# Kernel optimization log

Hardware: AMD Instinct MI355X
Metric: run time of the kernel (lower is better)

Reference implementation:

```python
import jax, jax.numpy as jnp
import numpy as np

EPS = 1e-12  # matches torch F.normalize default eps


def setup_inputs() -> dict:
    key = jax.random.key(0)
    k1, = jax.random.split(key, 1)
    N, M, D = 1024, 40, 768
    x = jax.random.normal(k1, (N, M, D), dtype=jnp.float32)
    w = jnp.asarray(15.0, dtype=jnp.float32)
    b = jnp.asarray(-7.0, dtype=jnp.float32)
    return {"x": x, "w": w, "b": b}


def reference(x, w, b):
    N, M, D = x.shape
    # L2 normalize along feature dim (torch F.normalize: x / max(||x||, eps))
    norm = jnp.linalg.norm(x, axis=-1, keepdims=True)
    xn = x / jnp.maximum(norm, EPS)
    # Inclusive centroids [N, D]
    c_incl = jnp.mean(xn, axis=1)
    # Exclusive centroids [N, M, D]: leave-one-out mean
    c_excl = (M * c_incl[:, None, :] - xn) / (M - 1)
    # Similarity of every utterance to every inclusive centroid: [N, M, N]
    sim = jnp.einsum('nmd,kd->nmk', xn, c_incl)
    # Own-speaker column uses the exclusive centroid instead (vectorized
    # replacement of the per-speaker diagonal-block loop)
    diag = jnp.sum(xn * c_excl, axis=-1)                 # [N, M]
    own = jnp.eye(N, dtype=bool)[:, None, :]             # [N, 1, N]
    sim = jnp.where(own, diag[:, :, None], sim)
    # Affine scale then cross-entropy against speaker labels
    logits = (w * sim + b).reshape(N * M, N)
    labels = jnp.repeat(jnp.arange(N), M)                # [N*M]
    lse = jax.nn.logsumexp(logits, axis=-1)
    picked = jnp.take_along_axis(logits, labels[:, None], axis=1)[:, 0]
    loss = jnp.mean(lse - picked)
    return loss
```

## Files before the change

kernel.cpp:

```cpp
#include <hip/hip_runtime.h>
#include <hip/hip_bf16.h>
#include <hip/hip_fp8.h>

typedef float f32x4 __attribute__((ext_vector_type(4)));
typedef long long i64;
typedef i64 i64x2 __attribute__((ext_vector_type(2)));

#define N_SPK 1024
#define M_UTT 40
#define D_FEAT 768
#define NROWS (N_SPK * M_UTT)
#define LOG2E 1.44269504088896340736f
#define LN2   0.69314718055994530942f

#define BM 128
#define BN 128
#define BKB 64
#define KT (D_FEAT / BKB)
#define ROWB 768

#define INV_SS (1.0f / 64.0f)
#define SCL 8.0f

__device__ __forceinline__ unsigned char to_fp8(float v) {
  __hip_fp8_e4m3 t(v);
  return (unsigned char)t.__x;
}


__global__ __launch_bounds__(256) void k_norm_cent(const float* __restrict__ x,
                                                   unsigned char* __restrict__ xn,
                                                   unsigned char* __restrict__ cc) {
  const int n = blockIdx.x, t = threadIdx.x;
  const float* xb = x + (size_t)n * (M_UTT * D_FEAT);
  unsigned char* ob = xn + (size_t)n * (M_UTT * D_FEAT);
  const int lane = t & 63, wv = t >> 6;
  const int j  = t & 63;
  const int pj = ((j >> 3) & 3) * 16 + (j & 7) + ((j >> 5) << 3);
  const int s0 = (t & ~63) + pj;
  __shared__ float wsum[2][2][4];
  float c0 = 0.f, c1 = 0.f, c2 = 0.f;
  for (int m = 0; m < M_UTT; m += 2) {
    const int p = (m >> 1) & 1;
    const float* r0 = xb + (size_t)m * D_FEAT;
    const float* r1 = r0 + D_FEAT;
    float a0 = r0[t], a1 = r0[t + 256], a2 = r0[t + 512];
    float b0 = r1[t], b1 = r1[t + 256], b2 = r1[t + 512];
    float sq0 = a0 * a0 + a1 * a1 + a2 * a2;
    float sq1 = b0 * b0 + b1 * b1 + b2 * b2;
#pragma unroll
    for (int d = 1; d < 64; d <<= 1) {
      sq0 += __shfl_xor(sq0, d, 64);
      sq1 += __shfl_xor(sq1, d, 64);
    }
    if (lane == 0) { wsum[p][0][wv] = sq0; wsum[p][1][wv] = sq1; }
    __syncthreads();
    const float t0 = wsum[p][0][0] + wsum[p][0][1] + wsum[p][0][2] + wsum[p][0][3];
    const float t1 = wsum[p][1][0] + wsum[p][1][1] + wsum[p][1][2] + wsum[p][1][3];
    const float i0 = 1.0f / fmaxf(sqrtf(t0), 1e-12f);
    const float i1 = 1.0f / fmaxf(sqrtf(t1), 1e-12f);
    a0 *= i0; a1 *= i0; a2 *= i0;
    b0 *= i1; b1 *= i1; b2 *= i1;
    unsigned char* o0 = ob + (size_t)m * D_FEAT;
    unsigned char* o1 = o0 + D_FEAT;
    o0[s0] = to_fp8(a0 * SCL); o0[s0 + 256] = to_fp8(a1 * SCL); o0[s0 + 512] = to_fp8(a2 * SCL);
    o1[s0] = to_fp8(b0 * SCL); o1[s0 + 256] = to_fp8(b1 * SCL); o1[s0 + 512] = to_fp8(b2 * SCL);
    c0 += a0 + b0; c1 += a1 + b1; c2 += a2 + b2;
  }
  unsigned char* co = cc + (size_t)n * D_FEAT;
  co[s0]       = to_fp8(c0 * (SCL / M_UTT));
  co[s0 + 256] = to_fp8(c1 * (SCL / M_UTT));
  co[s0 + 512] = to_fp8(c2 * (SCL / M_UTT));
}

#define GLD(g, l) __builtin_amdgcn_global_load_lds( \
    (const __attribute__((address_space(1))) unsigned int*)(g), \
    (__attribute__((address_space(3))) unsigned int*)(l), 16, 0, 0)

__global__ __launch_bounds__(256, 4) void k_gemm_part(
    const unsigned char* __restrict__ XN, const unsigned char* __restrict__ CC,
    const float* __restrict__ wp, const float* __restrict__ bp,
    float2* __restrict__ ppart, float* __restrict__ picked2) {

  __shared__ __align__(16) char smem[32768];

  const int tid  = threadIdx.x;
  const int wave = tid >> 6, lane = tid & 63;
  const int l16  = lane & 15, lg = lane >> 4;
  const int wr   = wave >> 1, wc = wave & 1;

  const int bid = blockIdx.x;
  const int xcd = bid & 7;
  const int tt  = bid >> 3;
  const int rb  = xcd * 40 + (tt >> 3);
  const int cb  = tt & 7;
  const int rowbase = rb * BM;
  const int colbase = cb * BN;

  const int R7   = (tid >> 3) & 7;
  const int li   = ((tid & 7) * 16) ^ (R7 << 4);
  const int row0 = 2 * (tid >> 3) + (li >> 6);
  const int kb   = li & 63;
  const int t16  = tid * 16;
  const unsigned char* gA = XN + (size_t)(rowbase + row0) * ROWB + kb;
  const unsigned char* gB = CC + (size_t)(colbase + row0) * ROWB + kb;

  const int xr  = ((l16 >> 1) & 7) << 4;
  const int in0 = ((((l16 & 1) << 6) | (lg << 4)) ^ xr);
  int aoff[4], boff[4];
#pragma unroll
  for (int i = 0; i < 4; ++i) {
    aoff[i] = (wr * 32 + i * 8 + (l16 >> 1)) * 128 + in0;
    boff[i] = 8192 + (wc * 32 + i * 8 + (l16 >> 1)) * 128 + in0;
  }

  f32x4 acc[4][4];
#pragma unroll
  for (int i = 0; i < 4; ++i)
#pragma unroll
    for (int jj = 0; jj < 4; ++jj) acc[i][jj] = (f32x4){0.f, 0.f, 0.f, 0.f};

  auto STAGE = [&](int buf, int koff) {
    char* sb = smem + buf * 16384;
    GLD(gA + koff,              sb + t16);
    GLD(gA + 64 * ROWB + koff,  sb + 4096 + t16);
    GLD(gB + koff,              sb + 8192 + t16);
    GLD(gB + 64 * ROWB + koff,  sb + 12288 + t16);
  };

  STAGE(0, 0);

  for (int k = 0; k < KT; ++k) {
    const char* bb = smem + (k & 1) * 16384;
    if (k + 1 < KT) {
      STAGE((k + 1) & 1, (k + 1) * BKB);
      asm volatile("s_waitcnt vmcnt(4)" ::: "memory");
    } else {
      asm volatile("s_waitcnt vmcnt(0)" ::: "memory");
    }
    __builtin_amdgcn_s_barrier();

    i64x2 av[4], bv[4];
#pragma unroll
    for (int i = 0; i < 4; ++i) av[i] = *(const i64x2*)(bb + aoff[i]);
#pragma unroll
    for (int jj = 0; jj < 4; ++jj) bv[jj] = *(const i64x2*)(bb + boff[jj]);
    __builtin_amdgcn_s_setprio(1);
#pragma unroll
    for (int i = 0; i < 4; ++i)
#pragma unroll
      for (int jj = 0; jj < 4; ++jj)
        acc[i][jj] = __builtin_amdgcn_mfma_f32_16x16x32_fp8_fp8(av[i][0], bv[jj][0], acc[i][jj], 0, 0, 0);
#pragma unroll
    for (int i = 0; i < 4; ++i)
#pragma unroll
      for (int jj = 0; jj < 4; ++jj)
        acc[i][jj] = __builtin_amdgcn_mfma_f32_16x16x32_fp8_fp8(av[i][1], bv[jj][1], acc[i][jj], 0, 0, 0);
    __builtin_amdgcn_s_setprio(0);
    asm volatile("s_waitcnt lgkmcnt(0)" ::: "memory");
    __builtin_amdgcn_s_barrier();
  }

  const float ws2 = wp[0] * LOG2E;
  const float b2  = bp[0] * LOG2E;
  float2* red = (float2*)smem;

#pragma unroll
  for (int i = 0; i < 4; ++i) {
#pragma unroll
    for (int rr = 0; rr < 4; ++rr) {
      const int lrow = wr * 64 + i * 16 + lg * 4 + rr;
      const int R = rowbase + lrow;
      const int n = R / M_UTT;
      float l2[4];
#pragma unroll
      for (int jj = 0; jj < 4; ++jj) {
        float sim = acc[i][jj][rr] * INV_SS;
        const int gc = colbase + wc * 64 + jj * 16 + l16;
        if (gc == n) {
          sim = (40.f * sim - 1.f) * (1.f / 39.f);
          picked2[R] = fmaf(ws2, sim, b2);
        }
        l2[jj] = fmaf(ws2, sim, b2);
      }
      float mx = fmaxf(fmaxf(l2[0], l2[1]), fmaxf(l2[2], l2[3]));
#pragma unroll
      for (int d = 1; d < 16; d <<= 1) mx = fmaxf(mx, __shfl_xor(mx, d, 64));
      float s = exp2f(l2[0] - mx) + exp2f(l2[1] - mx) +
                exp2f(l2[2] - mx) + exp2f(l2[3] - mx);
#pragma unroll
      for (int d = 1; d < 16; d <<= 1) s += __shfl_xor(s, d, 64);
      if (l16 == 0) red[lrow * 2 + wc] = make_float2(mx, s);
    }
  }
  __syncthreads();
  if (tid < 128) {
    const float2 p0 = red[tid * 2 + 0];
    const float2 p1 = red[tid * 2 + 1];
    const float m2 = fmaxf(p0.x, p1.x);
    const float ss = p0.y * exp2f(p0.x - m2) + p1.y * exp2f(p1.x - m2);
    ppart[(size_t)(rowbase + tid) * 8 + cb] = make_float2(m2, ss);
  }
}

__global__ __launch_bounds__(256) void k_combine(const float2* __restrict__ pp,
                                                 const float* __restrict__ picked2,
                                                 float* __restrict__ rowloss) {
  const int R = blockIdx.x * 256 + threadIdx.x;
  const float2* p = pp + (size_t)R * 8;
  float2 v[8];
#pragma unroll
  for (int j = 0; j < 8; ++j) v[j] = p[j];
  float m2 = v[0].x;
#pragma unroll
  for (int j = 1; j < 8; ++j) m2 = fmaxf(m2, v[j].x);
  float s = 0.f;
#pragma unroll
  for (int j = 0; j < 8; ++j) s += v[j].y * exp2f(v[j].x - m2);
  const float lse2 = m2 + log2f(s);
  rowloss[R] = (lse2 - picked2[R]) * LN2;
}

__global__ __launch_bounds__(512) void k_reduce(const float* __restrict__ rowloss,
                                                float* __restrict__ out) {
  const int t = threadIdx.x;
  double s = 0.0;
  for (int i = t; i < NROWS; i += 512) s += (double)rowloss[i];
  __shared__ double sm[512];
  sm[t] = s;
  __syncthreads();
  for (int off = 256; off > 0; off >>= 1) {
    if (t < off) sm[t] += sm[t + off];
    __syncthreads();
  }
  if (t == 0) out[0] = (float)(sm[0] / (double)NROWS);
}

extern "C" void kernel_launch(void* const* d_in, const int* in_sizes, int n_in,
                              void* d_out, int out_size, void* d_ws, size_t ws_size,
                              hipStream_t stream) {
  const float* x = (const float*)d_in[0];
  const float* w = (const float*)d_in[1];
  const float* b = (const float*)d_in[2];
  char* ws = (char*)d_ws;
  size_t off = 0;
  unsigned char* xn = (unsigned char*)(ws + off); off += (size_t)NROWS * D_FEAT;
  unsigned char* cc = (unsigned char*)(ws + off); off += (size_t)N_SPK * D_FEAT;
  off = (off + 255) & ~(size_t)255;
  float2* ppart      = (float2*)(ws + off);        off += (size_t)NROWS * 8 * sizeof(float2);
  float* picked2     = (float*)(ws + off);         off += (size_t)NROWS * sizeof(float);
  float* rowloss     = (float*)(ws + off);         off += (size_t)NROWS * sizeof(float);
  float* out = (float*)d_out;

  k_norm_cent<<<N_SPK, 256, 0, stream>>>(x, xn, cc);
  k_gemm_part<<<(NROWS / BM) * (N_SPK / BN), 256, 0, stream>>>(xn, cc, w, b, ppart, picked2);
  k_combine<<<NROWS / 256, 256, 0, stream>>>(ppart, picked2, rowloss);
  k_reduce<<<1, 512, 0, stream>>>(rowloss, out);
}
```

Baseline: 114.5 us.

## Switch GEMM to scaled 16x16x128 FP8 MFMA with 128-byte K tiles

Replaces pairs of 16x16x32 FP8 MFMAs with the gfx950 scaled 16x16x128 f8f6f4 MFMA using unit scales. The K tile doubles to 128 bytes and LDS grows to 64 KB with a new XOR swizzle, and the norm kernel now writes FP8 rows in natural order instead of pre-permuted. The goal is fewer MFMA issues, fewer loop iterations and fewer barriers. In exchange, occupancy drops from 4 to 2 blocks per CU, and the new layout and swizzle must stay consistent with the operand format the instruction expects.

After: 316.9 us. +176.8%, slower.

```diff
diff --git a/kernel.cpp b/kernel.cpp
--- a/kernel.cpp
+++ b/kernel.cpp
@@ -3,8 +3,8 @@
 #include <hip/hip_fp8.h>
 
 typedef float f32x4 __attribute__((ext_vector_type(4)));
-typedef long long i64;
-typedef i64 i64x2 __attribute__((ext_vector_type(2)));
+typedef int   i32x4 __attribute__((ext_vector_type(4)));
+typedef int   i32x8 __attribute__((ext_vector_type(8)));
 
 #define N_SPK 1024
 #define M_UTT 40
@@ -15,18 +15,18 @@
 
 #define BM 128
 #define BN 128
-#define BKB 64
+#define BKB 128
 #define KT (D_FEAT / BKB)
 #define ROWB 768
 
 #define INV_SS (1.0f / 64.0f)
 #define SCL 8.0f
+#define SCALE1 0x7F7F7F7F
 
 __device__ __forceinline__ unsigned char to_fp8(float v) {
   __hip_fp8_e4m3 t(v);
   return (unsigned char)t.__x;
 }
-
 
 __global__ __launch_bounds__(256) void k_norm_cent(const float* __restrict__ x,
                                                    unsigned char* __restrict__ xn,
@@ -35,9 +35,6 @@
   const float* xb = x + (size_t)n * (M_UTT * D_FEAT);
   unsigned char* ob = xn + (size_t)n * (M_UTT * D_FEAT);
   const int lane = t & 63, wv = t >> 6;
-  const int j  = t & 63;
-  const int pj = ((j >> 3) & 3) * 16 + (j & 7) + ((j >> 5) << 3);
-  const int s0 = (t & ~63) + pj;
   __shared__ float wsum[2][2][4];
   float c0 = 0.f, c1 = 0.f, c2 = 0.f;
   for (int m = 0; m < M_UTT; m += 2) {
@@ -63,26 +60,26 @@
     b0 *= i1; b1 *= i1; b2 *= i1;
     unsigned char* o0 = ob + (size_t)m * D_FEAT;
     unsigned char* o1 = o0 + D_FEAT;
-    o0[s0] = to_fp8(a0 * SCL); o0[s0 + 256] = to_fp8(a1 * SCL); o0[s0 + 512] = to_fp8(a2 * SCL);
-    o1[s0] = to_fp8(b0 * SCL); o1[s0 + 256] = to_fp8(b1 * SCL); o1[s0 + 512] = to_fp8(b2 * SCL);
+    o0[t] = to_fp8(a0 * SCL); o0[t + 256] = to_fp8(a1 * SCL); o0[t + 512] = to_fp8(a2 * SCL);
+    o1[t] = to_fp8(b0 * SCL); o1[t + 256] = to_fp8(b1 * SCL); o1[t + 512] = to_fp8(b2 * SCL);
     c0 += a0 + b0; c1 += a1 + b1; c2 += a2 + b2;
   }
   unsigned char* co = cc + (size_t)n * D_FEAT;
-  co[s0]       = to_fp8(c0 * (SCL / M_UTT));
-  co[s0 + 256] = to_fp8(c1 * (SCL / M_UTT));
-  co[s0 + 512] = to_fp8(c2 * (SCL / M_UTT));
+  co[t]       = to_fp8(c0 * (SCL / M_UTT));
+  co[t + 256] = to_fp8(c1 * (SCL / M_UTT));
+  co[t + 512] = to_fp8(c2 * (SCL / M_UTT));
 }
 
 #define GLD(g, l) __builtin_amdgcn_global_load_lds( \
     (const __attribute__((address_space(1))) unsigned int*)(g), \
     (__attribute__((address_space(3))) unsigned int*)(l), 16, 0, 0)
 
-__global__ __launch_bounds__(256, 4) void k_gemm_part(
+__global__ __launch_bounds__(256, 2) void k_gemm_part(
     const unsigned char* __restrict__ XN, const unsigned char* __restrict__ CC,
     const float* __restrict__ wp, const float* __restrict__ bp,
     float2* __restrict__ ppart, float* __restrict__ picked2) {
 
-  __shared__ __align__(16) char smem[32768];
+  __shared__ __align__(16) char smem[65536];
 
   const int tid  = threadIdx.x;
   const int wave = tid >> 6, lane = tid & 63;
@@ -97,21 +94,19 @@
   const int rowbase = rb * BM;
   const int colbase = cb * BN;
 
-  const int R7   = (tid >> 3) & 7;
-  const int li   = ((tid & 7) * 16) ^ (R7 << 4);
-  const int row0 = 2 * (tid >> 3) + (li >> 6);
-  const int kb   = li & 63;
+  const int row0 = tid >> 3;
+  const int u    = (tid & 7) ^ ((tid >> 3) & 7);
   const int t16  = tid * 16;
-  const unsigned char* gA = XN + (size_t)(rowbase + row0) * ROWB + kb;
-  const unsigned char* gB = CC + (size_t)(colbase + row0) * ROWB + kb;
-
-  const int xr  = ((l16 >> 1) & 7) << 4;
-  const int in0 = ((((l16 & 1) << 6) | (lg << 4)) ^ xr);
+  const unsigned char* gA = XN + (size_t)(rowbase + row0) * ROWB + u * 16;
+  const unsigned char* gB = CC + (size_t)(colbase + row0) * ROWB + u * 16;
+
+  const int m7 = l16 & 7;
+  const int s0 = ((2 * lg) ^ m7) << 4;
   int aoff[4], boff[4];
 #pragma unroll
   for (int i = 0; i < 4; ++i) {
-    aoff[i] = (wr * 32 + i * 8 + (l16 >> 1)) * 128 + in0;
-    boff[i] = 8192 + (wc * 32 + i * 8 + (l16 >> 1)) * 128 + in0;
+    aoff[i] = (wr * 64 + i * 16 + l16) * 128 + s0;
+    boff[i] = 16384 + (wc * 64 + i * 16 + l16) * 128 + s0;
   }
 
   f32x4 acc[4][4];
@@ -121,41 +116,47 @@
     for (int jj = 0; jj < 4; ++jj) acc[i][jj] = (f32x4){0.f, 0.f, 0.f, 0.f};
 
   auto STAGE = [&](int buf, int koff) {
-    char* sb = smem + buf * 16384;
-    GLD(gA + koff,              sb + t16);
-    GLD(gA + 64 * ROWB + koff,  sb + 4096 + t16);
-    GLD(gB + koff,              sb + 8192 + t16);
-    GLD(gB + 64 * ROWB + koff,  sb + 12288 + t16);
+    char* sb = smem + buf * 32768;
+#pragma unroll
+    for (int q = 0; q < 4; ++q)
+      GLD(gA + (size_t)q * (32 * ROWB) + koff, sb + q * 4096 + t16);
+#pragma unroll
+    for (int q = 0; q < 4; ++q)
+      GLD(gB + (size_t)q * (32 * ROWB) + koff, sb + 16384 + q * 4096 + t16);
   };
 
   STAGE(0, 0);
 
   for (int k = 0; k < KT; ++k) {
-    const char* bb = smem + (k & 1) * 16384;
+    const char* bb = smem + (k & 1) * 32768;
     if (k + 1 < KT) {
       STAGE((k + 1) & 1, (k + 1) * BKB);
-      asm volatile("s_waitcnt vmcnt(4)" ::: "memory");
+      asm volatile("s_waitcnt vmcnt(8)" ::: "memory");
     } else {
       asm volatile("s_waitcnt vmcnt(0)" ::: "memory");
     }
     __builtin_amdgcn_s_barrier();
 
-    i64x2 av[4], bv[4];
-#pragma unroll
-    for (int i = 0; i < 4; ++i) av[i] = *(const i64x2*)(bb + aoff[i]);
-#pragma unroll
-    for (int jj = 0; jj < 4; ++jj) bv[jj] = *(const i64x2*)(bb + boff[jj]);
+    i32x8 av[4], bv[4];
+#pragma unroll
+    for (int i = 0; i < 4; ++i) {
+      const i32x4 lo = *(const i32x4*)(bb + aoff[i]);
+      const i32x4 hi = *(const i32x4*)(bb + (aoff[i] ^ 16));
+      av[i] = __builtin_shufflevector(lo, hi, 0, 1, 2, 3, 4, 5, 6, 7);
+    }
+#pragma unroll
+    for (int jj = 0; jj < 4; ++jj) {
+      const i32x4 lo = *(const i32x4*)(bb + boff[jj]);
+      const i32x4 hi = *(const i32x4*)(bb + (boff[jj] ^ 16));
+      bv[jj] = __builtin_shufflevector(lo, hi, 0, 1, 2, 3, 4, 5, 6, 7);
+    }
     __builtin_amdgcn_s_setprio(1);
 #pragma unroll
     for (int i = 0; i < 4; ++i)
 #pragma unroll
       for (int jj = 0; jj < 4; ++jj)
-        acc[i][jj] = __builtin_amdgcn_mfma_f32_16x16x32_fp8_fp8(av[i][0], bv[jj][0], acc[i][jj], 0, 0, 0);
-#pragma unroll
-    for (int i = 0; i < 4; ++i)
-#pragma unroll
-      for (int jj = 0; jj < 4; ++jj)
-        acc[i][jj] = __builtin_amdgcn_mfma_f32_16x16x32_fp8_fp8(av[i][1], bv[jj][1], acc[i][jj], 0, 0, 0);
+        acc[i][jj] = __builtin_amdgcn_mfma_scale_f32_16x16x128_f8f6f4(
+            av[i], bv[jj], acc[i][jj], 0, 0, 0, SCALE1, 0, SCALE1);
     __builtin_amdgcn_s_setprio(0);
     asm volatile("s_waitcnt lgkmcnt(0)" ::: "memory");
     __builtin_amdgcn_s_barrier();
```

## Split GEMM tile across eight waves with 512-thread blocks

Applied to the files above, without the earlier changes.

Doubles the block to 512 threads so each of eight waves computes a 64x32 sub-tile instead of 64x64. Each thread now issues two async global-to-LDS loads per stage instead of four, and the epilogue merges four column partials per row instead of two. A fragments are loaded inside the MFMA loop. The aim is more resident waves to hide memory and LDS latency, at the cost of less A-fragment reuse per wave and more LDS reads per MFMA.

After: 123.9 us. +8.2%, slower.

```diff
diff --git a/kernel.cpp b/kernel.cpp
--- a/kernel.cpp
+++ b/kernel.cpp
@@ -77,7 +77,7 @@
     (const __attribute__((address_space(1))) unsigned int*)(g), \
     (__attribute__((address_space(3))) unsigned int*)(l), 16, 0, 0)
 
-__global__ __launch_bounds__(256, 4) void k_gemm_part(
+__global__ __launch_bounds__(512, 6) void k_gemm_part(
     const unsigned char* __restrict__ XN, const unsigned char* __restrict__ CC,
     const float* __restrict__ wp, const float* __restrict__ bp,
     float2* __restrict__ ppart, float* __restrict__ picked2) {
@@ -87,7 +87,8 @@
   const int tid  = threadIdx.x;
   const int wave = tid >> 6, lane = tid & 63;
   const int l16  = lane & 15, lg = lane >> 4;
-  const int wr   = wave >> 1, wc = wave & 1;
+  const int wr2  = wave >> 2;
+  const int wc4  = wave & 3;
 
   const int bid = blockIdx.x;
   const int xcd = bid & 7;
@@ -107,25 +108,24 @@
 
   const int xr  = ((l16 >> 1) & 7) << 4;
   const int in0 = ((((l16 & 1) << 6) | (lg << 4)) ^ xr);
-  int aoff[4], boff[4];
-#pragma unroll
-  for (int i = 0; i < 4; ++i) {
-    aoff[i] = (wr * 32 + i * 8 + (l16 >> 1)) * 128 + in0;
-    boff[i] = 8192 + (wc * 32 + i * 8 + (l16 >> 1)) * 128 + in0;
-  }
-
-  f32x4 acc[4][4];
+  int aoff[4], boff[2];
 #pragma unroll
   for (int i = 0; i < 4; ++i)
-#pragma unroll
-    for (int jj = 0; jj < 4; ++jj) acc[i][jj] = (f32x4){0.f, 0.f, 0.f, 0.f};
+    aoff[i] = (wr2 * 32 + i * 8 + (l16 >> 1)) * 128 + in0;
+#pragma unroll
+  for (int jj = 0; jj < 2; ++jj)
+    boff[jj] = 8192 + (wc4 * 16 + jj * 8 + (l16 >> 1)) * 128 + in0;
+
+  f32x4 acc[4][2];
+#pragma unroll
+  for (int i = 0; i < 4; ++i)
+#pragma unroll
+    for (int jj = 0; jj < 2; ++jj) acc[i][jj] = (f32x4){0.f, 0.f, 0.f, 0.f};
 
   auto STAGE = [&](int buf, int koff) {
     char* sb = smem + buf * 16384;
-    GLD(gA + koff,              sb + t16);
-    GLD(gA + 64 * ROWB + koff,  sb + 4096 + t16);
-    GLD(gB + koff,              sb + 8192 + t16);
-    GLD(gB + 64 * ROWB + koff,  sb + 12288 + t16);
+    GLD(gA + koff, sb + t16);
+    GLD(gB + koff, sb + 8192 + t16);
   };
 
   STAGE(0, 0);
@@ -134,28 +134,25 @@
     const char* bb = smem + (k & 1) * 16384;
     if (k + 1 < KT) {
       STAGE((k + 1) & 1, (k + 1) * BKB);
-      asm volatile("s_waitcnt vmcnt(4)" ::: "memory");
+      asm volatile("s_waitcnt vmcnt(2)" ::: "memory");
     } else {
       asm volatile("s_waitcnt vmcnt(0)" ::: "memory");
     }
     __builtin_amdgcn_s_barrier();
 
-    i64x2 av[4], bv[4];
-#pragma unroll
-    for (int i = 0; i < 4; ++i) av[i] = *(const i64x2*)(bb + aoff[i]);
-#pragma unroll
-    for (int jj = 0; jj < 4; ++jj) bv[jj] = *(const i64x2*)(bb + boff[jj]);
+    i64x2 bv[2];
+#pragma unroll
+    for (int jj = 0; jj < 2; ++jj) bv[jj] = *(const i64x2*)(bb + boff[jj]);
     __builtin_amdgcn_s_setprio(1);
 #pragma unroll
-    for (int i = 0; i < 4; ++i)
-#pragma unroll
-      for (int jj = 0; jj < 4; ++jj)
-        acc[i][jj] = __builtin_amdgcn_mfma_f32_16x16x32_fp8_fp8(av[i][0], bv[jj][0], acc[i][jj], 0, 0, 0);
-#pragma unroll
-    for (int i = 0; i < 4; ++i)
-#pragma unroll
-      for (int jj = 0; jj < 4; ++jj)
-        acc[i][jj] = __builtin_amdgcn_mfma_f32_16x16x32_fp8_fp8(av[i][1], bv[jj][1], acc[i][jj], 0, 0, 0);
+    for (int i = 0; i < 4; ++i) {
+      const i64x2 av = *(const i64x2*)(bb + aoff[i]);
+#pragma unroll
+      for (int jj = 0; jj < 2; ++jj) {
+        acc[i][jj] = __builtin_amdgcn_mfma_f32_16x16x32_fp8_fp8(av[0], bv[jj][0], acc[i][jj], 0, 0, 0);
+        acc[i][jj] = __builtin_amdgcn_mfma_f32_16x16x32_fp8_fp8(av[1], bv[jj][1], acc[i][jj], 0, 0, 0);
+      }
+    }
     __builtin_amdgcn_s_setprio(0);
     asm volatile("s_waitcnt lgkmcnt(0)" ::: "memory");
     __builtin_amdgcn_s_barrier();
@@ -169,36 +166,38 @@
   for (int i = 0; i < 4; ++i) {
 #pragma unroll
     for (int rr = 0; rr < 4; ++rr) {
-      const int lrow = wr * 64 + i * 16 + lg * 4 + rr;
+      const int lrow = wr2 * 64 + i * 16 + lg * 4 + rr;
       const int R = rowbase + lrow;
       const int n = R / M_UTT;
-      float l2[4];
-#pragma unroll
-      for (int jj = 0; jj < 4; ++jj) {
+      float l2[2];
+#pragma unroll
+      for (int jj = 0; jj < 2; ++jj) {
         float sim = acc[i][jj][rr] * INV_SS;
-        const int gc = colbase + wc * 64 + jj * 16 + l16;
+        const int gc = colbase + wc4 * 32 + jj * 16 + l16;
         if (gc == n) {
           sim = (40.f * sim - 1.f) * (1.f / 39.f);
           picked2[R] = fmaf(ws2, sim, b2);
         }
         l2[jj] = fmaf(ws2, sim, b2);
       }
-      float mx = fmaxf(fmaxf(l2[0], l2[1]), fmaxf(l2[2], l2[3]));
+      float mx = fmaxf(l2[0], l2[1]);
 #pragma unroll
       for (int d = 1; d < 16; d <<= 1) mx = fmaxf(mx, __shfl_xor(mx, d, 64));
-      float s = exp2f(l2[0] - mx) + exp2f(l2[1] - mx) +
-                exp2f(l2[2] - mx) + exp2f(l2[3] - mx);
+      float s = exp2f(l2[0] - mx) + exp2f(l2[1] - mx);
 #pragma unroll
       for (int d = 1; d < 16; d <<= 1) s += __shfl_xor(s, d, 64);
-      if (l16 == 0) red[lrow * 2 + wc] = make_float2(mx, s);
+      if (l16 == 0) red[lrow * 4 + wc4] = make_float2(mx, s);
     }
   }
   __syncthreads();
   if (tid < 128) {
-    const float2 p0 = red[tid * 2 + 0];
-    const float2 p1 = red[tid * 2 + 1];
-    const float m2 = fmaxf(p0.x, p1.x);
-    const float ss = p0.y * exp2f(p0.x - m2) + p1.y * exp2f(p1.x - m2);
+    const float2 v0 = red[tid * 4 + 0];
+    const float2 v1 = red[tid * 4 + 1];
+    const float2 v2 = red[tid * 4 + 2];
+    const float2 v3 = red[tid * 4 + 3];
+    const float m2 = fmaxf(fmaxf(v0.x, v1.x), fmaxf(v2.x, v3.x));
+    const float ss = v0.y * exp2f(v0.x - m2) + v1.y * exp2f(v1.x - m2) +
+                     v2.y * exp2f(v2.x - m2) + v3.y * exp2f(v3.x - m2);
     ppart[(size_t)(rowbase + tid) * 8 + cb] = make_float2(m2, ss);
   }
 }
@@ -253,7 +252,7 @@
   float* out = (float*)d_out;
 
   k_norm_cent<<<N_SPK, 256, 0, stream>>>(x, xn, cc);
-  k_gemm_part<<<(NROWS / BM) * (N_SPK / BN), 256, 0, stream>>>(xn, cc, w, b, ppart, picked2);
+  k_gemm_part<<<(NROWS / BM) * (N_SPK / BN), 512, 0, stream>>>(xn, cc, w, b, ppart, picked2);
   k_combine<<<NROWS / 256, 256, 0, stream>>>(ppart, picked2, rowloss);
   k_reduce<<<1, 512, 0, stream>>>(rowloss, out);
 }
```

## Vectorize normalize kernel with float4 loads and fold row-loss reduction into combine

Applied to the files above, without the earlier changes.

The normalization kernel now has each thread load float4 chunks covering four utterance rows per iteration. Norms are reduced through shared-memory bins, and the permuted fp8 output is written as uchar4. Centroid sums are combined across the four row slots in shared memory at the end. The combine kernel also does a per-block double reduction of the row losses, so the final reduce reads 160 partials instead of 40960 floats. This targets scalar memory traffic and fewer sync iterations in the bandwidth-bound first kernel, at the cost of more shared memory and index arithmetic.

Measured after the change: 95.12 us (median of 2 runs). 1.2x faster.

```diff
diff --git a/kernel.cpp b/kernel.cpp
--- a/kernel.cpp
+++ b/kernel.cpp
@@ -27,50 +27,91 @@
   return (unsigned char)t.__x;
 }
 
+__device__ __forceinline__ int perm4base(int k0) {
+  const int b = k0 & 63;
+  return (k0 & ~63) + ((b >> 3) & 3) * 16 + (b & 7) + ((b >> 5) << 3);
+}
 
 __global__ __launch_bounds__(256) void k_norm_cent(const float* __restrict__ x,
                                                    unsigned char* __restrict__ xn,
                                                    unsigned char* __restrict__ cc) {
   const int n = blockIdx.x, t = threadIdx.x;
-  const float* xb = x + (size_t)n * (M_UTT * D_FEAT);
+  const int lane = t & 63, wv = t >> 6;
+  const float4* xb4 = (const float4*)(x + (size_t)n * (M_UTT * D_FEAT));
   unsigned char* ob = xn + (size_t)n * (M_UTT * D_FEAT);
-  const int lane = t & 63, wv = t >> 6;
-  const int j  = t & 63;
-  const int pj = ((j >> 3) & 3) * 16 + (j & 7) + ((j >> 5) << 3);
-  const int s0 = (t & ~63) + pj;
-  __shared__ float wsum[2][2][4];
-  float c0 = 0.f, c1 = 0.f, c2 = 0.f;
-  for (int m = 0; m < M_UTT; m += 2) {
-    const int p = (m >> 1) & 1;
-    const float* r0 = xb + (size_t)m * D_FEAT;
-    const float* r1 = r0 + D_FEAT;
-    float a0 = r0[t], a1 = r0[t + 256], a2 = r0[t + 512];
-    float b0 = r1[t], b1 = r1[t + 256], b2 = r1[t + 512];
-    float sq0 = a0 * a0 + a1 * a1 + a2 * a2;
-    float sq1 = b0 * b0 + b1 * b1 + b2 * b2;
+
+  __shared__ float bins[2][4][3];
+  __shared__ float cl[4][192][4];
+
+  int o_[3], c4_[3], soff_[3];
+#pragma unroll
+  for (int q = 0; q < 3; ++q) {
+    const int f = q * 256 + t;
+    o_[q]  = f / 192;
+    c4_[q] = f % 192;
+    soff_[q] = perm4base(4 * c4_[q]);
+  }
+
+  float cacc[3][4];
+#pragma unroll
+  for (int q = 0; q < 3; ++q)
+#pragma unroll
+    for (int c = 0; c < 4; ++c) cacc[q][c] = 0.f;
+
+  for (int g = 0; g < M_UTT / 4; ++g) {
+    const int p = g & 1;
+    float4 v[3];
+#pragma unroll
+    for (int q = 0; q < 3; ++q) v[q] = xb4[g * 768 + q * 256 + t];
+    float ss[3];
+#pragma unroll
+    for (int q = 0; q < 3; ++q)
+      ss[q] = v[q].x * v[q].x + v[q].y * v[q].y + v[q].z * v[q].z + v[q].w * v[q].w;
 #pragma unroll
     for (int d = 1; d < 64; d <<= 1) {
-      sq0 += __shfl_xor(sq0, d, 64);
-      sq1 += __shfl_xor(sq1, d, 64);
-    }
-    if (lane == 0) { wsum[p][0][wv] = sq0; wsum[p][1][wv] = sq1; }
+      ss[0] += __shfl_xor(ss[0], d, 64);
+      ss[1] += __shfl_xor(ss[1], d, 64);
+      ss[2] += __shfl_xor(ss[2], d, 64);
+    }
+    if (lane == 0) {
+#pragma unroll
+      for (int q = 0; q < 3; ++q) {
+        const int idx = 4 * q + wv;
+        bins[p][idx / 3][idx % 3] = ss[q];
+      }
+    }
     __syncthreads();
-    const float t0 = wsum[p][0][0] + wsum[p][0][1] + wsum[p][0][2] + wsum[p][0][3];
-    const float t1 = wsum[p][1][0] + wsum[p][1][1] + wsum[p][1][2] + wsum[p][1][3];
-    const float i0 = 1.0f / fmaxf(sqrtf(t0), 1e-12f);
-    const float i1 = 1.0f / fmaxf(sqrtf(t1), 1e-12f);
-    a0 *= i0; a1 *= i0; a2 *= i0;
-    b0 *= i1; b1 *= i1; b2 *= i1;
-    unsigned char* o0 = ob + (size_t)m * D_FEAT;
-    unsigned char* o1 = o0 + D_FEAT;
-    o0[s0] = to_fp8(a0 * SCL); o0[s0 + 256] = to_fp8(a1 * SCL); o0[s0 + 512] = to_fp8(a2 * SCL);
-    o1[s0] = to_fp8(b0 * SCL); o1[s0 + 256] = to_fp8(b1 * SCL); o1[s0 + 512] = to_fp8(b2 * SCL);
-    c0 += a0 + b0; c1 += a1 + b1; c2 += a2 + b2;
-  }
-  unsigned char* co = cc + (size_t)n * D_FEAT;
-  co[s0]       = to_fp8(c0 * (SCL / M_UTT));
-  co[s0 + 256] = to_fp8(c1 * (SCL / M_UTT));
-  co[s0 + 512] = to_fp8(c2 * (SCL / M_UTT));
+#pragma unroll
+    for (int q = 0; q < 3; ++q) {
+      const int o = o_[q];
+      const float tot = bins[p][o][0] + bins[p][o][1] + bins[p][o][2];
+      const float iv = 1.0f / fmaxf(sqrtf(tot), 1e-12f);
+      const float w0 = v[q].x * iv, w1 = v[q].y * iv, w2 = v[q].z * iv, w3 = v[q].w * iv;
+      cacc[q][0] += w0; cacc[q][1] += w1; cacc[q][2] += w2; cacc[q][3] += w3;
+      uchar4 u;
+      u.x = to_fp8(w0 * SCL); u.y = to_fp8(w1 * SCL);
+      u.z = to_fp8(w2 * SCL); u.w = to_fp8(w3 * SCL);
+      *(uchar4*)(ob + (size_t)(4 * g + o) * D_FEAT + soff_[q]) = u;
+    }
+  }
+
+#pragma unroll
+  for (int q = 0; q < 3; ++q) {
+#pragma unroll
+    for (int c = 0; c < 4; ++c) cl[o_[q]][c4_[q]][c] = cacc[q][c];
+  }
+  __syncthreads();
+  if (t < 192) {
+    float s[4];
+#pragma unroll
+    for (int c = 0; c < 4; ++c)
+      s[c] = cl[0][t][c] + cl[1][t][c] + cl[2][t][c] + cl[3][t][c];
+    const float sc = SCL / (float)M_UTT;
+    uchar4 u;
+    u.x = to_fp8(s[0] * sc); u.y = to_fp8(s[1] * sc);
+    u.z = to_fp8(s[2] * sc); u.w = to_fp8(s[3] * sc);
+    *(uchar4*)(cc + (size_t)n * D_FEAT + perm4base(4 * t)) = u;
+  }
 }
 
 #define GLD(g, l) __builtin_amdgcn_global_load_lds( \
@@ -205,8 +246,9 @@
 
 __global__ __launch_bounds__(256) void k_combine(const float2* __restrict__ pp,
                                                  const float* __restrict__ picked2,
-                                                 float* __restrict__ rowloss) {
-  const int R = blockIdx.x * 256 + threadIdx.x;
+                                                 double* __restrict__ partial) {
+  const int t = threadIdx.x;
+  const int R = blockIdx.x * 256 + t;
   const float2* p = pp + (size_t)R * 8;
   float2 v[8];
 #pragma unroll
@@ -218,18 +260,25 @@
 #pragma unroll
   for (int j = 0; j < 8; ++j) s += v[j].y * exp2f(v[j].x - m2);
   const float lse2 = m2 + log2f(s);
-  rowloss[R] = (lse2 - picked2[R]) * LN2;
-}
-
-__global__ __launch_bounds__(512) void k_reduce(const float* __restrict__ rowloss,
+  const float rl = (lse2 - picked2[R]) * LN2;
+
+  __shared__ double sm[256];
+  sm[t] = (double)rl;
+  __syncthreads();
+  for (int off = 128; off > 0; off >>= 1) {
+    if (t < off) sm[t] += sm[t + off];
+    __syncthreads();
+  }
+  if (t == 0) partial[blockIdx.x] = sm[0];
+}
+
+__global__ __launch_bounds__(256) void k_reduce(const double* __restrict__ partial,
                                                 float* __restrict__ out) {
   const int t = threadIdx.x;
-  double s = 0.0;
-  for (int i = t; i < NROWS; i += 512) s += (double)rowloss[i];
-  __shared__ double sm[512];
-  sm[t] = s;
+  __shared__ double sm[256];
+  sm[t] = (t < NROWS / 256) ? partial[t] : 0.0;
   __syncthreads();
-  for (int off = 256; off > 0; off >>= 1) {
+  for (int off = 128; off > 0; off >>= 1) {
     if (t < off) sm[t] += sm[t + off];
     __syncthreads();
   }
@@ -247,13 +296,14 @@
   unsigned char* xn = (unsigned char*)(ws + off); off += (size_t)NROWS * D_FEAT;
   unsigned char* cc = (unsigned char*)(ws + off); off += (size_t)N_SPK * D_FEAT;
   off = (off + 255) & ~(size_t)255;
-  float2* ppart      = (float2*)(ws + off);        off += (size_t)NROWS * 8 * sizeof(float2);
-  float* picked2     = (float*)(ws + off);         off += (size_t)NROWS * sizeof(float);
-  float* rowloss     = (float*)(ws + off);         off += (size_t)NROWS * sizeof(float);
+  float2* ppart   = (float2*)(ws + off); off += (size_t)NROWS * 8 * sizeof(float2);
+  float* picked2  = (float*)(ws + off);  off += (size_t)NROWS * sizeof(float);
+  off = (off + 255) & ~(size_t)255;
+  double* partial = (double*)(ws + off); off += (size_t)(NROWS / 256) * sizeof(double);
   float* out = (float*)d_out;
 
   k_norm_cent<<<N_SPK, 256, 0, stream>>>(x, xn, cc);
   k_gemm_part<<<(NROWS / BM) * (N_SPK / BN), 256, 0, stream>>>(xn, cc, w, b, ppart, picked2);
-  k_combine<<<NROWS / 256, 256, 0, stream>>>(ppart, picked2, rowloss);
-  k_reduce<<<1, 512, 0, stream>>>(rowloss, out);
-}
+  k_combine<<<NROWS / 256, 256, 0, stream>>>(ppart, picked2, partial);
+  k_reduce<<<1, 256, 0, stream>>>(partial, out);
+}
```
